# Performance work log

Measured on AMD Instinct MI355X. Metric: run time of the kernel, lower is better.

The kernel has to match this reference:

```python
import jax, jax.numpy as jnp
import numpy as np

B, M, D = 8, 8192, 1024   # batch, tokens, latent_dim
N, P = 128, 1             # num_experts, slots_per_expert
F = 4096                  # expert_dim


def setup_inputs() -> dict:
    key = jax.random.key(0)
    k_x, k_phi, k_w1, k_b1, k_w2, k_b2 = jax.random.split(key, 6)
    x = jax.random.normal(k_x, (B, M, D), dtype=jnp.float32)
    # phi initialized as randn(d, n, p) / sqrt(d) in the original
    phi = jax.random.normal(k_phi, (D, N, P), dtype=jnp.float32) / (D ** 0.5)
    # Single shared expert MLP (original aliases one nn.Sequential across all experts)
    W1 = jax.random.normal(k_w1, (D, F), dtype=jnp.float32) / (D ** 0.5)
    b1 = jax.random.normal(k_b1, (F,), dtype=jnp.float32) * 0.01
    W2 = jax.random.normal(k_w2, (F, D), dtype=jnp.float32) / (F ** 0.5)
    b2 = jax.random.normal(k_b2, (D,), dtype=jnp.float32) * 0.01
    return {"x": x, "phi": phi, "W1": W1, "b1": b1, "W2": W2, "b2": b2}


def reference(x, phi, W1, b1, W2, b2):
    # dispatch / combine logits: [b, m, n, p]
    logits = jnp.einsum('bmd,dnp->bmnp', x, phi)
    d = jax.nn.softmax(logits, axis=1)                      # softmax over tokens m
    b_, m_, n_, p_ = logits.shape
    c = jax.nn.softmax(logits.reshape(b_, m_, n_ * p_), axis=-1).reshape(b_, m_, n_, p_)
    # slot inputs: [b, n, p, d]
    x_i = jnp.einsum('bmd,bmnp->bnpd', x, d)
    # shared expert MLP (torch GELU default = exact erf)
    h = jax.nn.gelu(jnp.einsum('bnpd,df->bnpf', x_i, W1) + b1, approximate=False)
    y_i = jnp.einsum('bnpf,fd->bnpd', h, W2) + b2
    # combine: [b, m, d]
    y = jnp.einsum('bnpd,bmnp->bmd', y_i, c)
    return y
```

## Files before the change

### kernel.cpp

```cpp
#include <hip/hip_runtime.h>
#include <math.h>

#define Bq 8
#define Mq 8192
#define Dq 1024
#define Nq 128
#define Fq 4096

typedef __bf16 bf16x8 __attribute__((ext_vector_type(8)));
typedef float f32x4 __attribute__((ext_vector_type(4)));
union P4 { __bf16 h[4]; unsigned long long u; };
union H8 { int4 v; _Float16 h[8]; };
union B8 { int4 v; __bf16 h[8]; };

__device__ __forceinline__ int swz128(int row, int bcol) {
  return row * 128 + (bcol ^ ((row & 7) << 4));
}
__device__ __forceinline__ int swz256(int row, int bcol) {
  return row * 256 + (bcol ^ ((row & 7) << 4));
}

__global__ __launch_bounds__(256) void wconv(const float* __restrict__ src,
                                             unsigned long long* __restrict__ dst, long n4)
{
  long i = (long)blockIdx.x * 256 + threadIdx.x;
  if (i >= n4) return;
  float4 v = ((const float4*)src)[i];
  P4 p; p.h[0] = (__bf16)v.x; p.h[1] = (__bf16)v.y; p.h[2] = (__bf16)v.z; p.h[3] = (__bf16)v.w;
  dst[i] = p.u;
}

__global__ __launch_bounds__(256) void logits_mfma(
    const float* __restrict__ x, const float* __restrict__ phi,
    __bf16* __restrict__ eT, __bf16* __restrict__ cbuf)
{
  __shared__ __align__(16) char sA[16384];
  __shared__ __align__(16) char sP[16384];
  int mt = blockIdx.x, b = blockIdx.y;
  int m0 = mt * 128;
  int t = threadIdx.x;
  int col = t & 127, half = t >> 7;
  int arow = t >> 4, ac4 = t & 15;
  int w = t >> 6, l = t & 63, la = l & 15, lb = l >> 4;

  f32x4 zero = {0.f, 0.f, 0.f, 0.f};
  f32x4 acc[2][8];
  for (int i = 0; i < 2; ++i) for (int j = 0; j < 8; ++j) acc[i][j] = zero;

  for (int k0 = 0; k0 < Dq; k0 += 64) {
    #pragma unroll
    for (int i = 0; i < 8; ++i) {
      int row = arow + 16 * i;
      float4 v = *(const float4*)(x + ((long)b * Mq + m0 + row) * Dq + k0 + ac4 * 4);
      P4 p;
      p.h[0] = (__bf16)v.x; p.h[1] = (__bf16)v.y;
      p.h[2] = (__bf16)v.z; p.h[3] = (__bf16)v.w;
      *(unsigned long long*)(sA + swz128(row, 8 * ac4)) = p.u;
    }
    {
      const float* Pp = phi + (long)(k0 + half * 32) * Nq + col;
      #pragma unroll
      for (int i = 0; i < 32; i += 4) {
        float a0 = Pp[(i + 0) * Nq], a1 = Pp[(i + 1) * Nq];
        float a2 = Pp[(i + 2) * Nq], a3 = Pp[(i + 3) * Nq];
        P4 p;
        p.h[0] = (__bf16)a0; p.h[1] = (__bf16)a1;
        p.h[2] = (__bf16)a2; p.h[3] = (__bf16)a3;
        *(unsigned long long*)(sP + swz128(col, 2 * (half * 32 + i))) = p.u;
      }
    }
    __syncthreads();
    #pragma unroll
    for (int sub = 0; sub < 2; ++sub) {
      int mbyte = sub * 64 + lb * 16;
      bf16x8 af0 = *(const bf16x8*)(sA + swz128(w * 32 + la, mbyte));
      bf16x8 af1 = *(const bf16x8*)(sA + swz128(w * 32 + 16 + la, mbyte));
      bf16x8 bv[8];
      #pragma unroll
      for (int j = 0; j < 8; ++j)
        bv[j] = *(const bf16x8*)(sP + swz128(j * 16 + la, mbyte));
      #pragma unroll
      for (int j = 0; j < 8; ++j) {
        acc[0][j] = __builtin_amdgcn_mfma_f32_16x16x32_bf16(af0, bv[j], acc[0][j], 0, 0, 0);
        acc[1][j] = __builtin_amdgcn_mfma_f32_16x16x32_bf16(af1, bv[j], acc[1][j], 0, 0, 0);
      }
    }
    __syncthreads();
  }
  float inv[2][4];
  #pragma unroll
  for (int i = 0; i < 2; ++i)
    #pragma unroll
    for (int r = 0; r < 4; ++r) {
      float s = 0.f;
      #pragma unroll
      for (int j = 0; j < 8; ++j) s += __expf(acc[i][j][r]);
      s += __shfl_xor(s, 1); s += __shfl_xor(s, 2);
      s += __shfl_xor(s, 4); s += __shfl_xor(s, 8);
      inv[i][r] = 1.0f / s;
    }
  __bf16* Cb = cbuf + ((long)b * Mq + m0) * Nq;
  __bf16* Eb = eT + (long)b * Nq * Mq + m0;
  #pragma unroll
  for (int i = 0; i < 2; ++i)
    #pragma unroll
    for (int j = 0; j < 8; ++j) {
      P4 p;
      #pragma unroll
      for (int r = 0; r < 4; ++r) {
        int row = w * 32 + i * 16 + lb * 4 + r;
        float e = __expf(acc[i][j][r]);
        p.h[r] = (__bf16)e;
        Cb[(long)row * Nq + j * 16 + la] = (__bf16)(e * inv[i][r]);
      }
      *(unsigned long long*)(Eb + (long)(j * 16 + la) * Mq + w * 32 + i * 16 + lb * 4) = p.u;
    }
}

__global__ __launch_bounds__(256) void colsum_rows(const __bf16* __restrict__ eT,
                                                   float* __restrict__ cinv)
{
  __shared__ float red[4];
  int r = blockIdx.x;
  int t = threadIdx.x;
  const __bf16* p = eT + (long)r * Mq;
  float s = 0.f;
  #pragma unroll
  for (int k = 0; k < 4; ++k) {
    B8 v; v.v = *(const int4*)(p + t * 8 + k * 2048);
    #pragma unroll
    for (int e = 0; e < 8; ++e) s += (float)v.h[e];
  }
  #pragma unroll
  for (int off = 32; off >= 1; off >>= 1) s += __shfl_down(s, off);
  if ((t & 63) == 0) red[t >> 6] = s;
  __syncthreads();
  if (t == 0) cinv[r] = 1.0f / (red[0] + red[1] + red[2] + red[3]);
}

__global__ __launch_bounds__(256) void xi_mfma(
    const __bf16* __restrict__ eT, const float* __restrict__ x,
    _Float16* __restrict__ part)
{
  __shared__ __align__(16) char sD[16384];
  __shared__ __align__(16) char sX[16384];
  int lin = blockIdx.x;
  int wk = (lin & 7) * 64 + (lin >> 3);
  int dts = wk & 7, kc = (wk >> 3) & 7, b = wk >> 6;
  int d0 = dts * 128;
  int t = threadIdx.x;
  int w = t >> 6, l = t & 63, la = l & 15, lb = l >> 4;
  int arow = t >> 1, ahalf = t & 1;
  const __bf16* Ep0 = eT + ((long)b * Nq + arow) * Mq + kc * 1024 + ahalf * 32;
  int bm = w * 2 + (l >> 5), bd = (l & 31) * 4;
  const float* Xp0 = x + ((long)b * Mq + kc * 1024 + bm) * Dq + d0 + bd;

  f32x4 zero = {0.f, 0.f, 0.f, 0.f};
  f32x4 acc[2][8];
  for (int i = 0; i < 2; ++i) for (int j = 0; j < 8; ++j) acc[i][j] = zero;

  int4 ar[4];
  float br[8][4];
  #pragma unroll
  for (int q = 0; q < 4; ++q) ar[q] = *(const int4*)(Ep0 + q * 8);
  #pragma unroll
  for (int k = 0; k < 8; ++k) *(float4*)br[k] = *(const float4*)(Xp0 + (long)k * 8 * Dq);
  #pragma unroll
  for (int q = 0; q < 4; ++q) *(int4*)(sD + swz128(arow, ahalf * 64 + q * 16)) = ar[q];
  #pragma unroll
  for (int k = 0; k < 8; ++k)
    #pragma unroll
    for (int q = 0; q < 4; ++q)
      *(__bf16*)(sX + swz128(bd + q, 2 * (k * 8 + bm))) = (__bf16)br[k][q];

  for (int it = 0; it < 16; ++it) {
    __syncthreads();
    if (it < 15) {
      #pragma unroll
      for (int q = 0; q < 4; ++q) ar[q] = *(const int4*)(Ep0 + (it + 1) * 64 + q * 8);
      #pragma unroll
      for (int k = 0; k < 8; ++k)
        *(float4*)br[k] = *(const float4*)(Xp0 + ((long)(it + 1) * 64 + k * 8) * Dq);
    }
    #pragma unroll
    for (int sub = 0; sub < 2; ++sub) {
      int mbyte = sub * 64 + lb * 16;
      bf16x8 af0 = *(const bf16x8*)(sD + swz128(w * 32 + la, mbyte));
      bf16x8 af1 = *(const bf16x8*)(sD + swz128(w * 32 + 16 + la, mbyte));
      #pragma unroll
      for (int j = 0; j < 8; ++j) {
        bf16x8 bv = *(const bf16x8*)(sX + swz128(j * 16 + la, mbyte));
        acc[0][j] = __builtin_amdgcn_mfma_f32_16x16x32_bf16(af0, bv, acc[0][j], 0, 0, 0);
        acc[1][j] = __builtin_amdgcn_mfma_f32_16x16x32_bf16(af1, bv, acc[1][j], 0, 0, 0);
      }
    }
    __syncthreads();
    if (it < 15) {
      #pragma unroll
      for (int q = 0; q < 4; ++q) *(int4*)(sD + swz128(arow, ahalf * 64 + q * 16)) = ar[q];
      #pragma unroll
      for (int k = 0; k < 8; ++k)
        #pragma unroll
        for (int q = 0; q < 4; ++q)
          *(__bf16*)(sX + swz128(bd + q, 2 * (k * 8 + bm))) = (__bf16)br[k][q];
    }
  }
  _Float16* P = part + ((long)kc * Bq + b) * (long)Nq * Dq + d0;
  #pragma unroll
  for (int i = 0; i < 2; ++i)
    #pragma unroll
    for (int j = 0; j < 8; ++j)
      #pragma unroll
      for (int r = 0; r < 4; ++r)
        P[(long)(w * 32 + i * 16 + lb * 4 + r) * Dq + j * 16 + la] = (_Float16)acc[i][j][r];
}

__global__ __launch_bounds__(256) void xi_reduce(const _Float16* __restrict__ part,
    const float* __restrict__ cinv, __bf16* __restrict__ xib)
{
  long base = ((long)blockIdx.x * 256 + threadIdx.x) * 8;
  int row = (int)(base >> 10);
  float civ = cinv[row];
  float s[8] = {};
  #pragma unroll
  for (int k = 0; k < 8; ++k) {
    H8 v; v.v = *(const int4*)(part + (long)k * 1048576 + base);
    #pragma unroll
    for (int e = 0; e < 8; ++e) s[e] += (float)v.h[e];
  }
  B8 o;
  #pragma unroll
  for (int e = 0; e < 8; ++e) o.h[e] = (__bf16)(s[e] * civ);
  *(int4*)(xib + base) = o.v;
}

template<int EPI, typename OT>
__global__ __launch_bounds__(256) void gemm_bf16(const __bf16* __restrict__ A,
    const __bf16* __restrict__ Bw, const float* __restrict__ bias,
    OT* __restrict__ C, int lda, int ldb, int ldc, int kLen, long strideCz)
{
  __shared__ __align__(16) char sA[16384];
  __shared__ __align__(16) char sB[16384];
  int m0 = blockIdx.x * 128, n0 = blockIdx.y * 128;
  int kbase = blockIdx.z * kLen;
  C += (long)blockIdx.z * strideCz;
  int t = threadIdx.x;
  int col = t & 127, half = t >> 7;
  int w = t >> 6, l = t & 63, la = l & 15, lb = l >> 4;

  f32x4 zero = {0.f, 0.f, 0.f, 0.f};
  f32x4 acc[2][8];
  for (int i = 0; i < 2; ++i) for (int j = 0; j < 8; ++j) acc[i][j] = zero;

  for (int kt = 0; kt < kLen; kt += 64) {
    int kp = kbase + kt;
    #pragma unroll
    for (int s = 0; s < 4; ++s) {
      int idx = t + 256 * s;
      int row = idx >> 3, c8 = idx & 7;
      *(int4*)(sA + swz128(row, c8 * 16)) =
          *(const int4*)(A + (long)(m0 + row) * lda + kp + c8 * 8);
    }
    {
      const __bf16* Bp = Bw + (long)(kp + half * 32) * ldb + n0 + col;
      #pragma unroll
      for (int i = 0; i < 32; i += 4) {
        P4 p;
        p.h[0] = Bp[(long)(i + 0) * ldb]; p.h[1] = Bp[(long)(i + 1) * ldb];
        p.h[2] = Bp[(long)(i + 2) * ldb]; p.h[3] = Bp[(long)(i + 3) * ldb];
        *(unsigned long long*)(sB + swz128(col, 2 * (half * 32 + i))) = p.u;
      }
    }
    __syncthreads();
    #pragma unroll
    for (int sub = 0; sub < 2; ++sub) {
      int mbyte = sub * 64 + lb * 16;
      bf16x8 af0 = *(const bf16x8*)(sA + swz128(w * 32 + la, mbyte));
      bf16x8 af1 = *(const bf16x8*)(sA + swz128(w * 32 + 16 + la, mbyte));
      bf16x8 bv[8];
      #pragma unroll
      for (int j = 0; j < 8; ++j)
        bv[j] = *(const bf16x8*)(sB + swz128(j * 16 + la, mbyte));
      #pragma unroll
      for (int j = 0; j < 8; ++j) {
        acc[0][j] = __builtin_amdgcn_mfma_f32_16x16x32_bf16(af0, bv[j], acc[0][j], 0, 0, 0);
        acc[1][j] = __builtin_amdgcn_mfma_f32_16x16x32_bf16(af1, bv[j], acc[1][j], 0, 0, 0);
      }
    }
    __syncthreads();
  }
  #pragma unroll
  for (int i = 0; i < 2; ++i)
    #pragma unroll
    for (int j = 0; j < 8; ++j)
      #pragma unroll
      for (int r = 0; r < 4; ++r) {
        int row = m0 + w * 32 + i * 16 + lb * 4 + r;
        int colg = n0 + j * 16 + la;
        float v = acc[i][j][r];
        if (EPI == 2) {
          v += bias[colg];
          v = 0.5f * v * (1.0f + erff(v * 0.70710678118654752f));
        }
        C[(long)row * ldc + colg] = (OT)v;
      }
}

__global__ __launch_bounds__(256) void g2_reduce(const float* __restrict__ part,
    const float* __restrict__ b2, __bf16* __restrict__ yiT)
{
  long idx = (long)blockIdx.x * 256 + threadIdx.x;
  int row = (int)(idx >> 10);
  int d = (int)(idx & 1023);
  float s = part[idx] + part[idx + 1048576] + part[idx + 2097152] + part[idx + 3145728] + b2[d];
  int b = row >> 7, n = row & 127;
  yiT[((long)b * Dq + d) * Nq + n] = (__bf16)s;
}

__global__ __launch_bounds__(256) void combine_mfma(const __bf16* __restrict__ cbuf,
    const __bf16* __restrict__ yiT, float* __restrict__ y)
{
  __shared__ __align__(16) char sC[32768];
  __shared__ __align__(16) char sY[32768];
  int lin = blockIdx.x;
  int wk = (lin & 7) * 512 + (lin >> 3);
  int dt = wk & 7, mt = (wk >> 3) & 63, b = wk >> 9;
  int m0 = mt * 128, d0 = dt * 128;
  int t = threadIdx.x;
  #pragma unroll
  for (int s = 0; s < 8; ++s) {
    int idx = t + 256 * s;
    int row = idx >> 4, c16 = idx & 15;
    *(int4*)(sC + swz256(row, c16 * 16)) =
        *(const int4*)(cbuf + ((long)b * Mq + m0 + row) * Nq + c16 * 8);
    *(int4*)(sY + swz256(row, c16 * 16)) =
        *(const int4*)(yiT + ((long)b * Dq + d0 + row) * Nq + c16 * 8);
  }
  __syncthreads();
  int w = t >> 6, l = t & 63, la = l & 15, lb = l >> 4;
  f32x4 zero = {0.f, 0.f, 0.f, 0.f};
  f32x4 acc[2][8];
  for (int i = 0; i < 2; ++i) for (int j = 0; j < 8; ++j) acc[i][j] = zero;
  #pragma unroll
  for (int sub = 0; sub < 4; ++sub) {
    int mbyte = sub * 64 + lb * 16;
    bf16x8 af0 = *(const bf16x8*)(sC + swz256(w * 32 + la, mbyte));
    bf16x8 af1 = *(const bf16x8*)(sC + swz256(w * 32 + 16 + la, mbyte));
    bf16x8 bv[8];
    #pragma unroll
    for (int j = 0; j < 8; ++j)
      bv[j] = *(const bf16x8*)(sY + swz256(j * 16 + la, mbyte));
    #pragma unroll
    for (int j = 0; j < 8; ++j) {
      acc[0][j] = __builtin_amdgcn_mfma_f32_16x16x32_bf16(af0, bv[j], acc[0][j], 0, 0, 0);
      acc[1][j] = __builtin_amdgcn_mfma_f32_16x16x32_bf16(af1, bv[j], acc[1][j], 0, 0, 0);
    }
  }
  float* Y = y + ((long)b * Mq + m0) * Dq + d0;
  #pragma unroll
  for (int i = 0; i < 2; ++i)
    #pragma unroll
    for (int j = 0; j < 8; ++j)
      #pragma unroll
      for (int r = 0; r < 4; ++r)
        Y[(long)(w * 32 + i * 16 + lb * 4 + r) * Dq + j * 16 + la] = acc[i][j][r];
}

extern "C" void kernel_launch(void* const* d_in, const int* in_sizes, int n_in,
                              void* d_out, int out_size, void* d_ws, size_t ws_size,
                              hipStream_t stream) {
  const float* x   = (const float*)d_in[0];
  const float* phi = (const float*)d_in[1];
  const float* W1  = (const float*)d_in[2];
  const float* b1  = (const float*)d_in[3];
  const float* W2  = (const float*)d_in[4];
  const float* b2  = (const float*)d_in[5];
  float* y = (float*)d_out;

  char* W = (char*)d_ws;
  __bf16*   cbuf   = (__bf16*)W;
  __bf16*   eT     = (__bf16*)(W + 16777216);
  __bf16*   h      = eT;
  _Float16* part   = (_Float16*)(W + 33554432);
  float*    g2part = (float*)(W + 33554432);
  __bf16*   W1b    = (__bf16*)(W + 50331648);
  __bf16*   W2b    = (__bf16*)(W + 58720256);
  __bf16*   xib    = (__bf16*)(W + 67108864);
  __bf16*   yiT    = (__bf16*)(W + 69206016);
  float*    cinv   = (float*)(W + 71303168);

  wconv<<<4096, 256, 0, stream>>>(W1, (unsigned long long*)W1b, 1048576);
  wconv<<<4096, 256, 0, stream>>>(W2, (unsigned long long*)W2b, 1048576);
  logits_mfma<<<dim3(Mq / 128, Bq), 256, 0, stream>>>(x, phi, eT, cbuf);
  colsum_rows<<<Bq * Nq, 256, 0, stream>>>(eT, cinv);
  xi_mfma<<<512, 256, 0, stream>>>(eT, x, part);
  xi_reduce<<<512, 256, 0, stream>>>(part, cinv, xib);
  gemm_bf16<2, __bf16><<<dim3(8, 32, 1), 256, 0, stream>>>(
      xib, W1b, b1, h, Dq, Fq, Fq, 1024, 0L);
  gemm_bf16<0, float><<<dim3(8, 8, 4), 256, 0, stream>>>(
      h, W2b, nullptr, g2part, Fq, Dq, Dq, 1024, 1048576L);
  g2_reduce<<<4096, 256, 0, stream>>>(g2part, b2, yiT);
  combine_mfma<<<4096, 256, 0, stream>>>(cbuf, yiT, y);
}
```

Before: 377.3 us.

## Emit transposed bf16 x in logits pass and loop d-tiles inside combine

The logits kernel now also writes a transposed bf16 copy of x from its shared-memory tile. A new xi kernel consumes that copy with register-prefetched double buffering instead of reading fp32 x. The combine kernel keeps each cbuf tile resident in shared memory and iterates over all d tiles, prefetching the next yiT tile, so cbuf is loaded once per block instead of eight times. The extra transposed write adds traffic and scalar LDS gathers to the logits kernel, and the larger combine blocks reduce grid parallelism.

```diff
diff --git a/kernel.cpp b/kernel.cpp
--- a/kernel.cpp
+++ b/kernel.cpp
@@ -30,9 +30,10 @@
   dst[i] = p.u;
 }
 
+template<bool WX>
 __global__ __launch_bounds__(256) void logits_mfma(
     const float* __restrict__ x, const float* __restrict__ phi,
-    __bf16* __restrict__ eT, __bf16* __restrict__ cbuf)
+    __bf16* __restrict__ eT, __bf16* __restrict__ cbuf, __bf16* __restrict__ xbT)
 {
   __shared__ __align__(16) char sA[16384];
   __shared__ __align__(16) char sP[16384];
@@ -85,6 +86,18 @@
         acc[1][j] = __builtin_amdgcn_mfma_f32_16x16x32_bf16(af1, bv[j], acc[1][j], 0, 0, 0);
       }
     }
+    if (WX) {
+      int dl = t >> 2, mg = t & 3;
+      __bf16* XT = xbT + ((long)b * Dq + k0 + dl) * Mq + m0 + mg * 32;
+      #pragma unroll
+      for (int q = 0; q < 4; ++q) {
+        B8 o;
+        #pragma unroll
+        for (int e = 0; e < 8; ++e)
+          o.h[e] = *(const __bf16*)(sA + swz128(mg * 32 + q * 8 + e, dl * 2));
+        *(int4*)(XT + q * 8) = o.v;
+      }
+    }
     __syncthreads();
   }
   float inv[2][4];
@@ -136,6 +149,78 @@
   if ((t & 63) == 0) red[t >> 6] = s;
   __syncthreads();
   if (t == 0) cinv[r] = 1.0f / (red[0] + red[1] + red[2] + red[3]);
+}
+
+__global__ __launch_bounds__(256) void xi_mfma_v2(
+    const __bf16* __restrict__ eT, const __bf16* __restrict__ xbT,
+    _Float16* __restrict__ part)
+{
+  __shared__ __align__(16) char sD[16384];
+  __shared__ __align__(16) char sX[16384];
+  int lin = blockIdx.x;
+  int wk = (lin & 7) * 64 + (lin >> 3);
+  int dts = wk & 7, kc = (wk >> 3) & 7, b = wk >> 6;
+  int d0 = dts * 128;
+  int t = threadIdx.x;
+  int w = t >> 6, l = t & 63, la = l & 15, lb = l >> 4;
+  int row = t >> 1, c8b = (t & 1) * 4;
+  const __bf16* Ep0 = eT + ((long)b * Nq + row) * Mq + kc * 1024 + c8b * 8;
+  const __bf16* Xp0 = xbT + ((long)b * Dq + d0 + row) * Mq + kc * 1024 + c8b * 8;
+
+  f32x4 zero = {0.f, 0.f, 0.f, 0.f};
+  f32x4 acc[2][8];
+  for (int i = 0; i < 2; ++i) for (int j = 0; j < 8; ++j) acc[i][j] = zero;
+
+  int4 ar[4], xr[4];
+  #pragma unroll
+  for (int q = 0; q < 4; ++q) {
+    ar[q] = *(const int4*)(Ep0 + q * 8);
+    xr[q] = *(const int4*)(Xp0 + q * 8);
+  }
+  #pragma unroll
+  for (int q = 0; q < 4; ++q) {
+    *(int4*)(sD + swz128(row, (c8b + q) * 16)) = ar[q];
+    *(int4*)(sX + swz128(row, (c8b + q) * 16)) = xr[q];
+  }
+
+  for (int it = 0; it < 16; ++it) {
+    __syncthreads();
+    if (it < 15) {
+      #pragma unroll
+      for (int q = 0; q < 4; ++q) {
+        ar[q] = *(const int4*)(Ep0 + (it + 1) * 64 + q * 8);
+        xr[q] = *(const int4*)(Xp0 + (it + 1) * 64 + q * 8);
+      }
+    }
+    #pragma unroll
+    for (int sub = 0; sub < 2; ++sub) {
+      int mbyte = sub * 64 + lb * 16;
+      bf16x8 af0 = *(const bf16x8*)(sD + swz128(w * 32 + la, mbyte));
+      bf16x8 af1 = *(const bf16x8*)(sD + swz128(w * 32 + 16 + la, mbyte));
+      #pragma unroll
+      for (int j = 0; j < 8; ++j) {
+        bf16x8 bv = *(const bf16x8*)(sX + swz128(j * 16 + la, mbyte));
+        acc[0][j] = __builtin_amdgcn_mfma_f32_16x16x32_bf16(af0, bv, acc[0][j], 0, 0, 0);
+        acc[1][j] = __builtin_amdgcn_mfma_f32_16x16x32_bf16(af1, bv, acc[1][j], 0, 0, 0);
+      }
+    }
+    __syncthreads();
+    if (it < 15) {
+      #pragma unroll
+      for (int q = 0; q < 4; ++q) {
+        *(int4*)(sD + swz128(row, (c8b + q) * 16)) = ar[q];
+        *(int4*)(sX + swz128(row, (c8b + q) * 16)) = xr[q];
+      }
+    }
+  }
+  _Float16* P = part + ((long)kc * Bq + b) * (long)Nq * Dq + d0;
+  #pragma unroll
+  for (int i = 0; i < 2; ++i)
+    #pragma unroll
+    for (int j = 0; j < 8; ++j)
+      #pragma unroll
+      for (int r = 0; r < 4; ++r)
+        P[(long)(w * 32 + i * 16 + lb * 4 + r) * Dq + j * 16 + la] = (_Float16)acc[i][j][r];
 }
 
 __global__ __launch_bounds__(256) void xi_mfma(
@@ -317,53 +402,65 @@
   yiT[((long)b * Dq + d) * Nq + n] = (__bf16)s;
 }
 
-__global__ __launch_bounds__(256) void combine_mfma(const __bf16* __restrict__ cbuf,
+__global__ __launch_bounds__(256) void combine_v2(const __bf16* __restrict__ cbuf,
     const __bf16* __restrict__ yiT, float* __restrict__ y)
 {
   __shared__ __align__(16) char sC[32768];
   __shared__ __align__(16) char sY[32768];
   int lin = blockIdx.x;
-  int wk = (lin & 7) * 512 + (lin >> 3);
-  int dt = wk & 7, mt = (wk >> 3) & 63, b = wk >> 9;
-  int m0 = mt * 128, d0 = dt * 128;
+  int wk = (lin & 7) * 64 + (lin >> 3);
+  int mt = wk & 63, b = wk >> 6;
+  int m0 = mt * 128;
   int t = threadIdx.x;
-  #pragma unroll
-  for (int s = 0; s < 8; ++s) {
-    int idx = t + 256 * s;
-    int row = idx >> 4, c16 = idx & 15;
+  int row = t >> 1, c16b = (t & 1) * 8;
+  #pragma unroll
+  for (int q = 0; q < 8; ++q) {
+    int c16 = c16b + q;
     *(int4*)(sC + swz256(row, c16 * 16)) =
         *(const int4*)(cbuf + ((long)b * Mq + m0 + row) * Nq + c16 * 8);
-    *(int4*)(sY + swz256(row, c16 * 16)) =
-        *(const int4*)(yiT + ((long)b * Dq + d0 + row) * Nq + c16 * 8);
-  }
-  __syncthreads();
+  }
+  const __bf16* Yb = yiT + ((long)b * Dq + row) * Nq + c16b * 8;
+  int4 yr[8];
+  #pragma unroll
+  for (int q = 0; q < 8; ++q) yr[q] = *(const int4*)(Yb + q * 8);
+
   int w = t >> 6, l = t & 63, la = l & 15, lb = l >> 4;
   f32x4 zero = {0.f, 0.f, 0.f, 0.f};
-  f32x4 acc[2][8];
-  for (int i = 0; i < 2; ++i) for (int j = 0; j < 8; ++j) acc[i][j] = zero;
-  #pragma unroll
-  for (int sub = 0; sub < 4; ++sub) {
-    int mbyte = sub * 64 + lb * 16;
-    bf16x8 af0 = *(const bf16x8*)(sC + swz256(w * 32 + la, mbyte));
-    bf16x8 af1 = *(const bf16x8*)(sC + swz256(w * 32 + 16 + la, mbyte));
-    bf16x8 bv[8];
-    #pragma unroll
-    for (int j = 0; j < 8; ++j)
-      bv[j] = *(const bf16x8*)(sY + swz256(j * 16 + la, mbyte));
-    #pragma unroll
-    for (int j = 0; j < 8; ++j) {
-      acc[0][j] = __builtin_amdgcn_mfma_f32_16x16x32_bf16(af0, bv[j], acc[0][j], 0, 0, 0);
-      acc[1][j] = __builtin_amdgcn_mfma_f32_16x16x32_bf16(af1, bv[j], acc[1][j], 0, 0, 0);
-    }
-  }
-  float* Y = y + ((long)b * Mq + m0) * Dq + d0;
-  #pragma unroll
-  for (int i = 0; i < 2; ++i)
-    #pragma unroll
-    for (int j = 0; j < 8; ++j)
-      #pragma unroll
-      for (int r = 0; r < 4; ++r)
-        Y[(long)(w * 32 + i * 16 + lb * 4 + r) * Dq + j * 16 + la] = acc[i][j][r];
+
+  for (int dt = 0; dt < 8; ++dt) {
+    #pragma unroll
+    for (int q = 0; q < 8; ++q)
+      *(int4*)(sY + swz256(row, (c16b + q) * 16)) = yr[q];
+    __syncthreads();
+    if (dt < 7) {
+      #pragma unroll
+      for (int q = 0; q < 8; ++q)
+        yr[q] = *(const int4*)(Yb + (long)(dt + 1) * 128 * Nq + q * 8);
+    }
+    f32x4 acc[2][8];
+    for (int i = 0; i < 2; ++i) for (int j = 0; j < 8; ++j) acc[i][j] = zero;
+    #pragma unroll
+    for (int sub = 0; sub < 4; ++sub) {
+      int mbyte = sub * 64 + lb * 16;
+      bf16x8 af0 = *(const bf16x8*)(sC + swz256(w * 32 + la, mbyte));
+      bf16x8 af1 = *(const bf16x8*)(sC + swz256(w * 32 + 16 + la, mbyte));
+      #pragma unroll
+      for (int j = 0; j < 8; ++j) {
+        bf16x8 bv = *(const bf16x8*)(sY + swz256(j * 16 + la, mbyte));
+        acc[0][j] = __builtin_amdgcn_mfma_f32_16x16x32_bf16(af0, bv, acc[0][j], 0, 0, 0);
+        acc[1][j] = __builtin_amdgcn_mfma_f32_16x16x32_bf16(af1, bv, acc[1][j], 0, 0, 0);
+      }
+    }
+    __syncthreads();
+    float* Y = y + ((long)b * Mq + m0) * Dq + dt * 128;
+    #pragma unroll
+    for (int i = 0; i < 2; ++i)
+      #pragma unroll
+      for (int j = 0; j < 8; ++j)
+        #pragma unroll
+        for (int r = 0; r < 4; ++r)
+          Y[(long)(w * 32 + i * 16 + lb * 4 + r) * Dq + j * 16 + la] = acc[i][j][r];
+  }
 }
 
 extern "C" void kernel_launch(void* const* d_in, const int* in_sizes, int n_in,
@@ -388,17 +485,23 @@
   __bf16*   xib    = (__bf16*)(W + 67108864);
   __bf16*   yiT    = (__bf16*)(W + 69206016);
   float*    cinv   = (float*)(W + 71303168);
+  __bf16*   xbT    = (__bf16*)(W + 75497472);
+  bool big = ws_size >= 209715200ull;
 
   wconv<<<4096, 256, 0, stream>>>(W1, (unsigned long long*)W1b, 1048576);
   wconv<<<4096, 256, 0, stream>>>(W2, (unsigned long long*)W2b, 1048576);
-  logits_mfma<<<dim3(Mq / 128, Bq), 256, 0, stream>>>(x, phi, eT, cbuf);
+  if (big)
+    logits_mfma<true><<<dim3(Mq / 128, Bq), 256, 0, stream>>>(x, phi, eT, cbuf, xbT);
+  else
+    logits_mfma<false><<<dim3(Mq / 128, Bq), 256, 0, stream>>>(x, phi, eT, cbuf, nullptr);
   colsum_rows<<<Bq * Nq, 256, 0, stream>>>(eT, cinv);
-  xi_mfma<<<512, 256, 0, stream>>>(eT, x, part);
+  if (big) xi_mfma_v2<<<512, 256, 0, stream>>>(eT, xbT, part);
+  else     xi_mfma<<<512, 256, 0, stream>>>(eT, x, part);
   xi_reduce<<<512, 256, 0, stream>>>(part, cinv, xib);
   gemm_bf16<2, __bf16><<<dim3(8, 32, 1), 256, 0, stream>>>(
       xib, W1b, b1, h, Dq, Fq, Fq, 1024, 0L);
   gemm_bf16<0, float><<<dim3(8, 8, 4), 256, 0, stream>>>(
       h, W2b, nullptr, g2part, Fq, Dq, Dq, 1024, 1048576L);
   g2_reduce<<<4096, 256, 0, stream>>>(g2part, b2, yiT);
-  combine_mfma<<<4096, 256, 0, stream>>>(cbuf, yiT, y);
-}
+  combine_v2<<<512, 256, 0, stream>>>(cbuf, yiT, y);
+}
```

New measurement: 478.4 us. 1.27x slower.

## Vectorize xi LDS stores, fragment-layout partials, and loop combine over D tiles

Applied to the files above, without the earlier changes.

The xi kernel now has each thread load 8 consecutive token rows, so it can pack them into one 16-byte LDS store instead of 32 scalar bf16 stores. The swizzle is also extended with row>>3 bits to reduce bank conflicts. Partial sums are written in MFMA fragment order as short4 vectors, and xi_reduce is rewritten to read that layout and scatter into xib. The combine kernel now keeps one cbuf tile in LDS and loops over all 8 D tiles, prefetching yiT through registers, which cuts redundant cbuf loads at the cost of fewer blocks (512) and extra syncs.

```diff
diff --git a/kernel.cpp b/kernel.cpp
--- a/kernel.cpp
+++ b/kernel.cpp
@@ -10,11 +10,11 @@
 typedef __bf16 bf16x8 __attribute__((ext_vector_type(8)));
 typedef float f32x4 __attribute__((ext_vector_type(4)));
 union P4 { __bf16 h[4]; unsigned long long u; };
-union H8 { int4 v; _Float16 h[8]; };
+union H4 { short4 v; _Float16 h[4]; };
 union B8 { int4 v; __bf16 h[8]; };
 
 __device__ __forceinline__ int swz128(int row, int bcol) {
-  return row * 128 + (bcol ^ ((row & 7) << 4));
+  return row * 128 + (bcol ^ ((((row & 7) ^ ((row >> 3) & 7))) << 4));
 }
 __device__ __forceinline__ int swz256(int row, int bcol) {
   return row * 256 + (bcol ^ ((row & 7) << 4));
@@ -152,8 +152,9 @@
   int w = t >> 6, l = t & 63, la = l & 15, lb = l >> 4;
   int arow = t >> 1, ahalf = t & 1;
   const __bf16* Ep0 = eT + ((long)b * Nq + arow) * Mq + kc * 1024 + ahalf * 32;
-  int bm = w * 2 + (l >> 5), bd = (l & 31) * 4;
-  const float* Xp0 = x + ((long)b * Mq + kc * 1024 + bm) * Dq + d0 + bd;
+  int bmb = (w * 2 + (l >> 5)) * 8;
+  int bd  = (l & 31) * 4;
+  const float* Xp0 = x + ((long)b * Mq + kc * 1024 + bmb) * Dq + d0 + bd;
 
   f32x4 zero = {0.f, 0.f, 0.f, 0.f};
   f32x4 acc[2][8];
@@ -164,14 +165,16 @@
   #pragma unroll
   for (int q = 0; q < 4; ++q) ar[q] = *(const int4*)(Ep0 + q * 8);
   #pragma unroll
-  for (int k = 0; k < 8; ++k) *(float4*)br[k] = *(const float4*)(Xp0 + (long)k * 8 * Dq);
+  for (int k = 0; k < 8; ++k) *(float4*)br[k] = *(const float4*)(Xp0 + (long)k * Dq);
   #pragma unroll
   for (int q = 0; q < 4; ++q) *(int4*)(sD + swz128(arow, ahalf * 64 + q * 16)) = ar[q];
   #pragma unroll
-  for (int k = 0; k < 8; ++k)
-    #pragma unroll
-    for (int q = 0; q < 4; ++q)
-      *(__bf16*)(sX + swz128(bd + q, 2 * (k * 8 + bm))) = (__bf16)br[k][q];
+  for (int q = 0; q < 4; ++q) {
+    B8 o;
+    #pragma unroll
+    for (int k = 0; k < 8; ++k) o.h[k] = (__bf16)br[k][q];
+    *(int4*)(sX + swz128(bd + q, 2 * bmb)) = o.v;
+  }
 
   for (int it = 0; it < 16; ++it) {
     __syncthreads();
@@ -180,7 +183,7 @@
       for (int q = 0; q < 4; ++q) ar[q] = *(const int4*)(Ep0 + (it + 1) * 64 + q * 8);
       #pragma unroll
       for (int k = 0; k < 8; ++k)
-        *(float4*)br[k] = *(const float4*)(Xp0 + ((long)(it + 1) * 64 + k * 8) * Dq);
+        *(float4*)br[k] = *(const float4*)(Xp0 + ((long)(it + 1) * 64 + k) * Dq);
     }
     #pragma unroll
     for (int sub = 0; sub < 2; ++sub) {
@@ -199,39 +202,48 @@
       #pragma unroll
       for (int q = 0; q < 4; ++q) *(int4*)(sD + swz128(arow, ahalf * 64 + q * 16)) = ar[q];
       #pragma unroll
-      for (int k = 0; k < 8; ++k)
+      for (int q = 0; q < 4; ++q) {
+        B8 o;
         #pragma unroll
-        for (int q = 0; q < 4; ++q)
-          *(__bf16*)(sX + swz128(bd + q, 2 * (k * 8 + bm))) = (__bf16)br[k][q];
-    }
-  }
-  _Float16* P = part + ((long)kc * Bq + b) * (long)Nq * Dq + d0;
+        for (int k = 0; k < 8; ++k) o.h[k] = (__bf16)br[k][q];
+        *(int4*)(sX + swz128(bd + q, 2 * bmb)) = o.v;
+      }
+    }
+  }
+  _Float16* P = part + (((long)kc * Bq + b) * 8 + dts) * 16384;
   #pragma unroll
   for (int i = 0; i < 2; ++i)
     #pragma unroll
-    for (int j = 0; j < 8; ++j)
-      #pragma unroll
-      for (int r = 0; r < 4; ++r)
-        P[(long)(w * 32 + i * 16 + lb * 4 + r) * Dq + j * 16 + la] = (_Float16)acc[i][j][r];
+    for (int j = 0; j < 8; ++j) {
+      H4 o;
+      #pragma unroll
+      for (int r = 0; r < 4; ++r) o.h[r] = (_Float16)acc[i][j][r];
+      *(short4*)(P + ((w * 16 + i * 8 + j) * 64 + l) * 4) = o.v;
+    }
 }
 
 __global__ __launch_bounds__(256) void xi_reduce(const _Float16* __restrict__ part,
     const float* __restrict__ cinv, __bf16* __restrict__ xib)
 {
-  long base = ((long)blockIdx.x * 256 + threadIdx.x) * 8;
-  int row = (int)(base >> 10);
-  float civ = cinv[row];
-  float s[8] = {};
-  #pragma unroll
-  for (int k = 0; k < 8; ++k) {
-    H8 v; v.v = *(const int4*)(part + (long)k * 1048576 + base);
-    #pragma unroll
-    for (int e = 0; e < 8; ++e) s[e] += (float)v.h[e];
-  }
-  B8 o;
-  #pragma unroll
-  for (int e = 0; e < 8; ++e) o.h[e] = (__bf16)(s[e] * civ);
-  *(int4*)(xib + base) = o.v;
+  int s = blockIdx.x * 256 + threadIdx.x;
+  int l = s & 63, j = (s >> 6) & 7, i = (s >> 9) & 1;
+  int w = (s >> 10) & 3, dts = (s >> 12) & 7, b = s >> 15;
+  const _Float16* p = part + ((long)b * 8 + dts) * 16384 + ((w * 16 + i * 8 + j) * 64 + l) * 4;
+  float sum[4] = {};
+  #pragma unroll
+  for (int kc = 0; kc < 8; ++kc) {
+    H4 v; v.v = *(const short4*)(p + (long)kc * 1048576);
+    #pragma unroll
+    for (int r = 0; r < 4; ++r) sum[r] += (float)v.h[r];
+  }
+  int lb = l >> 4, la = l & 15;
+  int nbase = w * 32 + i * 16 + lb * 4;
+  int d = dts * 128 + j * 16 + la;
+  #pragma unroll
+  for (int r = 0; r < 4; ++r) {
+    int n = b * 128 + nbase + r;
+    xib[(long)n * Dq + d] = (__bf16)(sum[r] * cinv[n]);
+  }
 }
 
 template<int EPI, typename OT>
@@ -317,53 +329,65 @@
   yiT[((long)b * Dq + d) * Nq + n] = (__bf16)s;
 }
 
-__global__ __launch_bounds__(256) void combine_mfma(const __bf16* __restrict__ cbuf,
+__global__ __launch_bounds__(256) void combine_v2(const __bf16* __restrict__ cbuf,
     const __bf16* __restrict__ yiT, float* __restrict__ y)
 {
   __shared__ __align__(16) char sC[32768];
   __shared__ __align__(16) char sY[32768];
   int lin = blockIdx.x;
-  int wk = (lin & 7) * 512 + (lin >> 3);
-  int dt = wk & 7, mt = (wk >> 3) & 63, b = wk >> 9;
-  int m0 = mt * 128, d0 = dt * 128;
+  int wk = (lin & 7) * 64 + (lin >> 3);
+  int mt = wk & 63, b = wk >> 6;
+  int m0 = mt * 128;
   int t = threadIdx.x;
-  #pragma unroll
-  for (int s = 0; s < 8; ++s) {
-    int idx = t + 256 * s;
-    int row = idx >> 4, c16 = idx & 15;
+  int row = t >> 1, c16b = (t & 1) * 8;
+  #pragma unroll
+  for (int q = 0; q < 8; ++q) {
+    int c16 = c16b + q;
     *(int4*)(sC + swz256(row, c16 * 16)) =
         *(const int4*)(cbuf + ((long)b * Mq + m0 + row) * Nq + c16 * 8);
-    *(int4*)(sY + swz256(row, c16 * 16)) =
-        *(const int4*)(yiT + ((long)b * Dq + d0 + row) * Nq + c16 * 8);
-  }
-  __syncthreads();
+  }
+  const __bf16* Yb = yiT + ((long)b * Dq + row) * Nq + c16b * 8;
+  int4 yr[8];
+  #pragma unroll
+  for (int q = 0; q < 8; ++q) yr[q] = *(const int4*)(Yb + q * 8);
+
   int w = t >> 6, l = t & 63, la = l & 15, lb = l >> 4;
   f32x4 zero = {0.f, 0.f, 0.f, 0.f};
-  f32x4 acc[2][8];
-  for (int i = 0; i < 2; ++i) for (int j = 0; j < 8; ++j) acc[i][j] = zero;
-  #pragma unroll
-  for (int sub = 0; sub < 4; ++sub) {
-    int mbyte = sub * 64 + lb * 16;
-    bf16x8 af0 = *(const bf16x8*)(sC + swz256(w * 32 + la, mbyte));
-    bf16x8 af1 = *(const bf16x8*)(sC + swz256(w * 32 + 16 + la, mbyte));
-    bf16x8 bv[8];
-    #pragma unroll
-    for (int j = 0; j < 8; ++j)
-      bv[j] = *(const bf16x8*)(sY + swz256(j * 16 + la, mbyte));
-    #pragma unroll
-    for (int j = 0; j < 8; ++j) {
-      acc[0][j] = __builtin_amdgcn_mfma_f32_16x16x32_bf16(af0, bv[j], acc[0][j], 0, 0, 0);
-      acc[1][j] = __builtin_amdgcn_mfma_f32_16x16x32_bf16(af1, bv[j], acc[1][j], 0, 0, 0);
-    }
-  }
-  float* Y = y + ((long)b * Mq + m0) * Dq + d0;
-  #pragma unroll
-  for (int i = 0; i < 2; ++i)
-    #pragma unroll
-    for (int j = 0; j < 8; ++j)
-      #pragma unroll
-      for (int r = 0; r < 4; ++r)
-        Y[(long)(w * 32 + i * 16 + lb * 4 + r) * Dq + j * 16 + la] = acc[i][j][r];
+
+  for (int dt = 0; dt < 8; ++dt) {
+    #pragma unroll
+    for (int q = 0; q < 8; ++q)
+      *(int4*)(sY + swz256(row, (c16b + q) * 16)) = yr[q];
+    __syncthreads();
+    if (dt < 7) {
+      #pragma unroll
+      for (int q = 0; q < 8; ++q)
+        yr[q] = *(const int4*)(Yb + (long)(dt + 1) * 128 * Nq + q * 8);
+    }
+    f32x4 acc[2][8];
+    for (int i = 0; i < 2; ++i) for (int j = 0; j < 8; ++j) acc[i][j] = zero;
+    #pragma unroll
+    for (int sub = 0; sub < 4; ++sub) {
+      int mbyte = sub * 64 + lb * 16;
+      bf16x8 af0 = *(const bf16x8*)(sC + swz256(w * 32 + la, mbyte));
+      bf16x8 af1 = *(const bf16x8*)(sC + swz256(w * 32 + 16 + la, mbyte));
+      #pragma unroll
+      for (int j = 0; j < 8; ++j) {
+        bf16x8 bv = *(const bf16x8*)(sY + swz256(j * 16 + la, mbyte));
+        acc[0][j] = __builtin_amdgcn_mfma_f32_16x16x32_bf16(af0, bv, acc[0][j], 0, 0, 0);
+        acc[1][j] = __builtin_amdgcn_mfma_f32_16x16x32_bf16(af1, bv, acc[1][j], 0, 0, 0);
+      }
+    }
+    __syncthreads();
+    float* Y = y + ((long)b * Mq + m0) * Dq + dt * 128;
+    #pragma unroll
+    for (int i = 0; i < 2; ++i)
+      #pragma unroll
+      for (int j = 0; j < 8; ++j)
+        #pragma unroll
+        for (int r = 0; r < 4; ++r)
+          Y[(long)(w * 32 + i * 16 + lb * 4 + r) * Dq + j * 16 + la] = acc[i][j][r];
+  }
 }
 
 extern "C" void kernel_launch(void* const* d_in, const int* in_sizes, int n_in,
@@ -394,11 +418,11 @@
   logits_mfma<<<dim3(Mq / 128, Bq), 256, 0, stream>>>(x, phi, eT, cbuf);
   colsum_rows<<<Bq * Nq, 256, 0, stream>>>(eT, cinv);
   xi_mfma<<<512, 256, 0, stream>>>(eT, x, part);
-  xi_reduce<<<512, 256, 0, stream>>>(part, cinv, xib);
+  xi_reduce<<<1024, 256, 0, stream>>>(part, cinv, xib);
   gemm_bf16<2, __bf16><<<dim3(8, 32, 1), 256, 0, stream>>>(
       xib, W1b, b1, h, Dq, Fq, Fq, 1024, 0L);
   gemm_bf16<0, float><<<dim3(8, 8, 4), 256, 0, stream>>>(
       h, W2b, nullptr, g2part, Fq, Dq, Dq, 1024, 1048576L);
   g2_reduce<<<4096, 256, 0, stream>>>(g2part, b2, yiT);
-  combine_mfma<<<4096, 256, 0, stream>>>(cbuf, yiT, y);
-}
+  combine_v2<<<512, 256, 0, stream>>>(cbuf, yiT, y);
+}
```

After: 404.9 us. 1.07x slower.
